# Performance work log

Measured on AMD Instinct MI355X. Metric: run time of the kernel, lower is better.

## Reference

```python
import jax, jax.numpy as jnp
import numpy as np
import math

CHUNK = 64

def _linear(x, W, b):
    # torch nn.Linear: y = x @ W.T + b
    return jnp.einsum('bsd,ed->bse', x, W) + b

def setup_inputs() -> dict:
    key = jax.random.key(0)
    ks = jax.random.split(key, 10)
    B, S, D = 4, 4096, 512
    scale = 0.02
    inp = {
        'x': jax.random.normal(ks[0], (B, S, D), jnp.float32),
        'base_phases': jax.random.normal(ks[1], (S, D), jnp.float32) * math.pi,
        'Wk': jax.random.normal(ks[2], (D, D), jnp.float32) * scale,
        'bk': jnp.zeros((D,), jnp.float32),
        'Wv': jax.random.normal(ks[3], (D, D), jnp.float32) * scale,
        'bv': jnp.zeros((D,), jnp.float32),
        'Wq': jax.random.normal(ks[4], (D, D), jnp.float32) * scale,
        'bq': jnp.zeros((D,), jnp.float32),
        'Wkm': jax.random.normal(ks[5], (D, D), jnp.float32) * scale,
        'bkm': jnp.zeros((D,), jnp.float32),
        'Wqm': jax.random.normal(ks[6], (D, D), jnp.float32) * scale,
        'bqm': jnp.zeros((D,), jnp.float32),
        'mod_scale': jnp.ones((1,), jnp.float32) * 0.1,
        'ln_g': jnp.ones((D,), jnp.float32),
        'ln_b': jnp.zeros((D,), jnp.float32),
        'Wo': jax.random.normal(ks[7], (D, D), jnp.float32) * scale,
        'bo': jnp.zeros((D,), jnp.float32),
    }
    return inp

def reference(x, base_phases, Wk, bk, Wv, bv, Wq, bq, Wkm, bkm, Wqm, bqm, mod_scale, ln_g, ln_b, Wo, bo):
    B, S, D = x.shape
    bp = base_phases[:S][None]                      # [1,S,D]
    key = _linear(x, Wk, bk)
    value = _linear(x, Wv, bv)
    query = _linear(x, Wq, bq)
    key_phase = bp + _linear(key, Wkm, bkm) * mod_scale
    query_phase = bp + _linear(query, Wqm, bqm) * mod_scale
    bound_real = value * jnp.cos(key_phase)
    bound_imag = value * jnp.sin(key_phase)
    # chunked cumulative memory (S divisible by CHUNK -> no padding)
    nC = S // CHUNK
    br = bound_real.reshape(B, nC, CHUNK, D)
    bi = bound_imag.reshape(B, nC, CHUNK, D)
    qp = query_phase.reshape(B, nC, CHUNK, D)
    mem_real = jnp.cumsum(br, axis=2)
    mem_imag = jnp.cumsum(bi, axis=2)
    retrieved = (mem_real * jnp.cos(qp) + mem_imag * jnp.sin(qp)).reshape(B, S, D)
    retrieved = retrieved / math.sqrt(D)
    # LayerNorm + Linear (to_out)
    mu = jnp.mean(retrieved, axis=-1, keepdims=True)
    var = jnp.mean((retrieved - mu) ** 2, axis=-1, keepdims=True)
    normed = (retrieved - mu) / jnp.sqrt(var + 1e-5) * ln_g + ln_b
    out = _linear(normed, Wo, bo)
    return x + out
```

## Files before the change

### kernel.cpp

```cpp
#include <hip/hip_runtime.h>
#include <hip/hip_bf16.h>


typedef __attribute__((ext_vector_type(8))) short short8;
typedef __attribute__((ext_vector_type(4))) float f32x4;

#define M_TOK   16384
#define DIM     512
#define NCHUNK  64
#define RPAD    520

__device__ __forceinline__ void gll16(const void* g, void* l) {
  __builtin_amdgcn_global_load_lds(
      (const __attribute__((address_space(1))) unsigned int*)g,
      (__attribute__((address_space(3))) unsigned int*)l, 16, 0, 0);
}

__device__ __forceinline__ uint2 pack4bf(float4 v) {
  union { __hip_bfloat16 h[4]; uint2 u; } t;
  t.h[0] = __float2bfloat16(v.x);
  t.h[1] = __float2bfloat16(v.y);
  t.h[2] = __float2bfloat16(v.z);
  t.h[3] = __float2bfloat16(v.w);
  return t.u;
}

__device__ __forceinline__ unsigned int pack2bf(float a, float b) {
  union { __hip_bfloat16 h[2]; unsigned int u; } t;
  t.h[0] = __float2bfloat16(a);
  t.h[1] = __float2bfloat16(b);
  return t.u;
}

__device__ __forceinline__ float u2f(unsigned short u) {
  union { unsigned int i; float f; } t;
  t.i = (unsigned int)u << 16;
  return t.f;
}

__global__ __launch_bounds__(256) void prep_all(
    const float* __restrict__ x, __hip_bfloat16* __restrict__ x_bf,
    const float* __restrict__ Wv, const float* __restrict__ Wo,
    const float* __restrict__ bv,
    const float* __restrict__ Wkm, const float* __restrict__ Wqm,
    const float* __restrict__ Wk, const float* __restrict__ Wq,
    const float* __restrict__ bk, const float* __restrict__ bkm,
    const float* __restrict__ bq, const float* __restrict__ bqm,
    __hip_bfloat16* __restrict__ Wall, float* __restrict__ bc1,
    __hip_bfloat16* __restrict__ Wm_bf, __hip_bfloat16* __restrict__ WT_bf) {
  const int tid = threadIdx.x;
  if (blockIdx.x < 8192) {
    int i = blockIdx.x * 256 + tid;
    ((uint2*)x_bf)[i] = pack4bf(((const float4*)x)[i]);
    return;
  }
  const int b = blockIdx.x - 8192;
  if (b < 512) {
    int m = b >> 8;
    int idx = ((b & 255) * 256 + tid) * 4;
    const float* src = m ? Wo : Wv;
    __hip_bfloat16* dst = Wall + (m ? (size_t)1536 * 512 : 0);
    ((uint2*)dst)[idx >> 2] = pack4bf(*(const float4*)(src + idx));
    int t = b * 256 + tid;
    if (t < 512) bc1[t] = bv[t];
  } else if (b < 1024) {
    int bb = b - 512;
    int m = bb >> 8;
    int idx = ((bb & 255) * 256 + tid) * 4;
    const float* src = m ? Wqm : Wkm;
    ((uint2*)(Wm_bf + (size_t)m * 262144))[idx >> 2] =
        pack4bf(*(const float4*)(src + idx));
  } else if (b < 1152) {
    __shared__ float tile[64][65];
    int bb = b - 1024;
    int z = bb >> 6;
    int tl = bb & 63;
    int tr = tl >> 3, tc = tl & 7;
    const float* src = z ? Wq : Wk;
#pragma unroll
    for (int i = 0; i < 4; i++) {
      int r = (tid >> 4) + 16 * i;
      int c4 = (tid & 15) * 4;
      float4 v = *(const float4*)(src + (size_t)(tr * 64 + r) * 512 +
                                  tc * 64 + c4);
      tile[r][c4 + 0] = v.x;
      tile[r][c4 + 1] = v.y;
      tile[r][c4 + 2] = v.z;
      tile[r][c4 + 3] = v.w;
    }
    __syncthreads();
    int orow = tid >> 2;
    int seg = tid & 3;
    __hip_bfloat16* dst = WT_bf + (size_t)z * 262144 +
                          (size_t)(tc * 64 + orow) * 512 + tr * 64 + seg * 16;
#pragma unroll
    for (int q = 0; q < 4; q++) {
      float4 v;
      v.x = tile[seg * 16 + q * 4 + 0][orow];
      v.y = tile[seg * 16 + q * 4 + 1][orow];
      v.z = tile[seg * 16 + q * 4 + 2][orow];
      v.w = tile[seg * 16 + q * 4 + 3][orow];
      *(uint2*)(dst + q * 4) = pack4bf(v);
    }
  } else {
    int row = (b - 1152) * 4 + (tid >> 6);
    int lane = tid & 63;
    int z = row >> 9;
    int i = row & 511;
    const float* Wm = z ? Wqm : Wkm;
    const float* b0 = z ? bq : bk;
    const float* bm = z ? bqm : bkm;
    const float4* w4 = (const float4*)(Wm + (size_t)i * 512 + lane * 8);
    const float4* v4 = (const float4*)(b0 + lane * 8);
    float4 w0 = w4[0], w1 = w4[1], c0 = v4[0], c1 = v4[1];
    float acc = w0.x * c0.x + w0.y * c0.y + w0.z * c0.z + w0.w * c0.w +
                w1.x * c1.x + w1.y * c1.y + w1.z * c1.z + w1.w * c1.w;
#pragma unroll
    for (int off = 32; off; off >>= 1) acc += __shfl_xor(acc, off, 64);
    if (lane == 0) bc1[512 + z * 512 + i] = acc + bm[i];
  }
}

__global__ __launch_bounds__(256) void gemm_bt(
    const __hip_bfloat16* __restrict__ A, int lda,
    const __hip_bfloat16* __restrict__ Bt,
    const float* __restrict__ bias,
    __hip_bfloat16* __restrict__ Cout, int ldc) {
  constexpr int K = 512, BK = 32;
  __shared__ __align__(16) __hip_bfloat16 As[2][128 * BK];
  __shared__ __align__(16) __hip_bfloat16 Bs[2][128 * BK];

  const int tid  = threadIdx.x;
  const int lane = tid & 63;
  const int w    = tid >> 6;
  const int wm   = w >> 1;
  const int wn   = w & 1;
  const int lb = (blockIdx.x & 7) * 192 + (blockIdx.x >> 3);
  const int by = lb / 12;
  const int bx = lb - by * 12;
  const int m0 = by * 128;
  const int n0 = bx * 128;

  const int rS0    = (w * 2 + 0) * 16 + (lane >> 2);
  const int rS1    = (w * 2 + 1) * 16 + (lane >> 2);
  const int kInRow = (lane & 3) * 8;
  const __hip_bfloat16* gA0 = A + (size_t)(m0 + rS0) * lda + kInRow;
  const __hip_bfloat16* gA1 = A + (size_t)(m0 + rS1) * lda + kInRow;
  const __hip_bfloat16* gB0 = Bt + (size_t)(n0 + rS0) * K + kInRow;
  const __hip_bfloat16* gB1 = Bt + (size_t)(n0 + rS1) * K + kInRow;
  char* ldsA0 = (char*)&As[0][0] + (w * 2 + 0) * 1024;
  char* ldsA1 = (char*)&As[0][0] + (w * 2 + 1) * 1024;
  char* ldsB0 = (char*)&Bs[0][0] + (w * 2 + 0) * 1024;
  char* ldsB1 = (char*)&Bs[0][0] + (w * 2 + 1) * 1024;

  f32x4 acc[4][4] = {};

  const int rfA = lane & 15;
  const int rfK = (lane >> 4) * 8;

  for (int kt = 0; kt < K; kt += 2 * BK) {
    __syncthreads();
    gll16(gA0 + kt, ldsA0);
    gll16(gA1 + kt, ldsA1);
    gll16(gB0 + kt, ldsB0);
    gll16(gB1 + kt, ldsB1);
    gll16(gA0 + kt + BK, ldsA0 + 8192);
    gll16(gA1 + kt + BK, ldsA1 + 8192);
    gll16(gB0 + kt + BK, ldsB0 + 8192);
    gll16(gB1 + kt + BK, ldsB1 + 8192);
    __syncthreads();

#pragma unroll
    for (int h = 0; h < 2; h++) {
      const __hip_bfloat16* Ah = &As[h][0];
      const __hip_bfloat16* Bh = &Bs[h][0];
      short8 af[4], bfv[4];
#pragma unroll
      for (int i = 0; i < 4; i++)
        af[i] = *(const short8*)(Ah + (wm * 64 + i * 16 + rfA) * BK + rfK);
#pragma unroll
      for (int j = 0; j < 4; j++)
        bfv[j] = *(const short8*)(Bh + (wn * 64 + j * 16 + rfA) * BK + rfK);
#pragma unroll
      for (int i = 0; i < 4; i++)
#pragma unroll
        for (int j = 0; j < 4; j++)
          acc[i][j] = __builtin_amdgcn_mfma_f32_16x16x32_bf16(
              af[i], bfv[j], acc[i][j], 0, 0, 0);
    }
  }

  const int cq = lane >> 4;
#pragma unroll
  for (int i = 0; i < 4; i++) {
    int row = m0 + wm * 64 + i * 16 + cq * 4;
#pragma unroll
    for (int j = 0; j < 4; j++) {
      int col = n0 + wn * 64 + j * 16 + (lane & 15);
      float bz = bias[col];
#pragma unroll
      for (int r = 0; r < 4; r++) {
        float v = acc[i][j][r] + bz;
        Cout[(size_t)(row + r) * ldc + col] = __float2bfloat16(v);
      }
    }
  }
}

__global__ __launch_bounds__(256) void gemm_compose(
    const __hip_bfloat16* __restrict__ Wm_bf,
    const __hip_bfloat16* __restrict__ WT_bf,
    __hip_bfloat16* __restrict__ Wall) {
  constexpr int K = 512, BK = 32;
  const __hip_bfloat16* A  = Wm_bf + (size_t)blockIdx.z * 262144;
  const __hip_bfloat16* Bt = WT_bf + (size_t)blockIdx.z * 262144;
  __hip_bfloat16* C = Wall + (size_t)(512 + blockIdx.z * 512) * 512;
  __shared__ __align__(16) __hip_bfloat16 As[128 * BK];
  __shared__ __align__(16) __hip_bfloat16 Bs[128 * BK];

  const int tid  = threadIdx.x;
  const int lane = tid & 63;
  const int w    = tid >> 6;
  const int wm   = w >> 1;
  const int wn   = w & 1;
  const int m0   = blockIdx.y * 128;
  const int n0   = blockIdx.x * 128;

  const int rS0    = (w * 2 + 0) * 16 + (lane >> 2);
  const int rS1    = (w * 2 + 1) * 16 + (lane >> 2);
  const int kInRow = (lane & 3) * 8;
  const __hip_bfloat16* gA0 = A + (size_t)(m0 + rS0) * K + kInRow;
  const __hip_bfloat16* gA1 = A + (size_t)(m0 + rS1) * K + kInRow;
  const __hip_bfloat16* gB0 = Bt + (size_t)(n0 + rS0) * K + kInRow;
  const __hip_bfloat16* gB1 = Bt + (size_t)(n0 + rS1) * K + kInRow;
  char* ldsA0 = (char*)As + (w * 2 + 0) * 1024;
  char* ldsA1 = (char*)As + (w * 2 + 1) * 1024;
  char* ldsB0 = (char*)Bs + (w * 2 + 0) * 1024;
  char* ldsB1 = (char*)Bs + (w * 2 + 1) * 1024;

  f32x4 acc[4][4] = {};
  const int rfA = lane & 15;
  const int rfK = (lane >> 4) * 8;

  for (int kt = 0; kt < K; kt += BK) {
    __syncthreads();
    gll16(gA0 + kt, ldsA0);
    gll16(gA1 + kt, ldsA1);
    gll16(gB0 + kt, ldsB0);
    gll16(gB1 + kt, ldsB1);
    __syncthreads();

    short8 af[4], bf[4];
#pragma unroll
    for (int i = 0; i < 4; i++)
      af[i] = *(const short8*)(As + (wm * 64 + i * 16 + rfA) * BK + rfK);
#pragma unroll
    for (int j = 0; j < 4; j++)
      bf[j] = *(const short8*)(Bs + (wn * 64 + j * 16 + rfA) * BK + rfK);
#pragma unroll
    for (int i = 0; i < 4; i++)
#pragma unroll
      for (int j = 0; j < 4; j++)
        acc[i][j] = __builtin_amdgcn_mfma_f32_16x16x32_bf16(
            af[i], bf[j], acc[i][j], 0, 0, 0);
  }

  const int cq = lane >> 4;
#pragma unroll
  for (int i = 0; i < 4; i++) {
    int row = m0 + wm * 64 + i * 16 + cq * 4;
#pragma unroll
    for (int j = 0; j < 4; j++) {
      int col = n0 + wn * 64 + j * 16 + (lane & 15);
#pragma unroll
      for (int r = 0; r < 4; r++)
        C[(size_t)(row + r) * 512 + col] = __float2bfloat16(acc[i][j][r]);
    }
  }
}

__global__ __launch_bounds__(1024) void fused_pg(
    const __hip_bfloat16* __restrict__ VKQ,
    const float* __restrict__ bp,
    const float* __restrict__ mod_scale,
    const float* __restrict__ ln_g, const float* __restrict__ ln_b,
    const __hip_bfloat16* __restrict__ WoB,
    const float* __restrict__ bo,
    const float* __restrict__ x,
    float* __restrict__ out) {
  __shared__ __hip_bfloat16 R[64 * RPAD];
  __shared__ float Tr[3][512], Ti[3][512];
  const int tid    = threadIdx.x;
  const int seg    = tid >> 8;
  const int d0     = (tid & 255) * 2;
  const int blk    = blockIdx.x;
  const int token0 = blk * 64;
  const int sg0    = (blk & (NCHUNK - 1)) * 64;
  const float msc  = mod_scale[0];
  const float isd  = 0.044194173824159216f;

  float cqs0[16], sqs0[16], cqs1[16], sqs1[16];

  {
    const int r0 = seg * 16;
    float mr0 = 0.f, mi0 = 0.f, mr1 = 0.f, mi1 = 0.f;
    const __hip_bfloat16* vb = VKQ + (size_t)(token0 + r0) * 1536 + d0;
    const float* bb = bp + (size_t)(sg0 + r0) * 512 + d0;
#pragma unroll
    for (int s = 0; s < 16; ++s) {
      ushort2 v2  = *(const ushort2*)(vb + (size_t)s * 1536);
      ushort2 km2 = *(const ushort2*)(vb + (size_t)s * 1536 + 512);
      ushort2 qm2 = *(const ushort2*)(vb + (size_t)s * 1536 + 1024);
      float2 b2   = *(const float2*)(bb + (size_t)s * 512);
      float v0 = u2f((unsigned short)v2.x), v1 = u2f((unsigned short)v2.y);
      float kp0 = b2.x + u2f((unsigned short)km2.x) * msc;
      float kp1 = b2.y + u2f((unsigned short)km2.y) * msc;
      float qp0 = b2.x + u2f((unsigned short)qm2.x) * msc;
      float qp1 = b2.y + u2f((unsigned short)qm2.y) * msc;
      float sk0, ck0, sk1, ck1, sq0, cq0, sq1, cq1;
      __sincosf(kp0, &sk0, &ck0);
      __sincosf(kp1, &sk1, &ck1);
      __sincosf(qp0, &sq0, &cq0);
      __sincosf(qp1, &sq1, &cq1);
      mr0 += v0 * ck0; mi0 += v0 * sk0;
      mr1 += v1 * ck1; mi1 += v1 * sk1;
      cqs0[s] = cq0; sqs0[s] = sq0;
      cqs1[s] = cq1; sqs1[s] = sq1;
      float rr0 = (mr0 * cq0 + mi0 * sq0) * isd;
      float rr1 = (mr1 * cq1 + mi1 * sq1) * isd;
      *(unsigned int*)(&R[(r0 + s) * RPAD + d0]) = pack2bf(rr0, rr1);
    }
    if (seg < 3) {
      Tr[seg][d0] = mr0; Tr[seg][d0 + 1] = mr1;
      Ti[seg][d0] = mi0; Ti[seg][d0 + 1] = mi1;
    }
  }
  __syncthreads();

  if (seg) {
    float pr0 = Tr[0][d0],     pi0 = Ti[0][d0];
    float pr1 = Tr[0][d0 + 1], pi1 = Ti[0][d0 + 1];
    if (seg >= 2) {
      pr0 += Tr[1][d0];     pi0 += Ti[1][d0];
      pr1 += Tr[1][d0 + 1]; pi1 += Ti[1][d0 + 1];
    }
    if (seg == 3) {
      pr0 += Tr[2][d0];     pi0 += Ti[2][d0];
      pr1 += Tr[2][d0 + 1]; pi1 += Ti[2][d0 + 1];
    }
    pr0 *= isd; pi0 *= isd; pr1 *= isd; pi1 *= isd;
    const int r0 = seg * 16;
#pragma unroll
    for (int s = 0; s < 16; ++s) {
      unsigned int* p = (unsigned int*)(&R[(r0 + s) * RPAD + d0]);
      unsigned int old = *p;
      float a = u2f((unsigned short)(old & 0xffffu)) +
                pr0 * cqs0[s] + pi0 * sqs0[s];
      float b = u2f((unsigned short)(old >> 16)) +
                pr1 * cqs1[s] + pi1 * sqs1[s];
      *p = pack2bf(a, b);
    }
  }
  __syncthreads();

  const int lane = tid & 63;
  const int wv   = tid >> 6;
  float xv[4][2][4];

  {
    float gj[8], bj[8];
#pragma unroll
    for (int j = 0; j < 8; j++) {
      int col = lane + 64 * j;
      gj[j] = ln_g[col];
      bj[j] = ln_b[col];
    }
    {
      const int cq_ = lane >> 4;
      const int c0  = lane & 15;
#pragma unroll
      for (int i = 0; i < 4; i++)
#pragma unroll
        for (int j = 0; j < 2; j++)
#pragma unroll
          for (int r = 0; r < 4; r++)
            xv[i][j][r] = x[(size_t)(token0 + i * 16 + cq_ * 4 + r) * 512 +
                            wv * 32 + j * 16 + c0];
    }
    for (int rr = 0; rr < 4; ++rr) {
      int row = wv * 4 + rr;
      float vals[8], sum = 0.f, sq2 = 0.f;
#pragma unroll
      for (int j = 0; j < 8; j++) {
        float v = u2f(*(const unsigned short*)&R[row * RPAD + lane + 64 * j]);
        vals[j] = v;
        sum += v;
        sq2 += v * v;
      }
#pragma unroll
      for (int off = 32; off; off >>= 1) {
        sum += __shfl_xor(sum, off, 64);
        sq2 += __shfl_xor(sq2, off, 64);
      }
      float mu   = sum * (1.f / 512.f);
      float var  = sq2 * (1.f / 512.f) - mu * mu;
      float rstd = rsqrtf(var + 1e-5f);
#pragma unroll
      for (int j = 0; j < 8; j++) {
        float nv = (vals[j] - mu) * rstd * gj[j] + bj[j];
        R[row * RPAD + lane + 64 * j] = __float2bfloat16(nv);
      }
    }
  }
  __syncthreads();

  {
    const int rfA = lane & 15;
    const int rfK = (lane >> 4) * 8;
    f32x4 acc[4][2] = {};

    for (int kt = 0; kt < 512; kt += 32) {
      short8 af[4], bfv[2];
#pragma unroll
      for (int j = 0; j < 2; j++) {
        int col = wv * 32 + j * 16 + rfA;
        bfv[j] = *(const short8*)(WoB + (size_t)col * 512 + kt + rfK);
      }
#pragma unroll
      for (int i = 0; i < 4; i++)
        af[i] = *(const short8*)(R + (i * 16 + rfA) * RPAD + kt + rfK);
#pragma unroll
      for (int i = 0; i < 4; i++)
#pragma unroll
        for (int j = 0; j < 2; j++)
          acc[i][j] = __builtin_amdgcn_mfma_f32_16x16x32_bf16(
              af[i], bfv[j], acc[i][j], 0, 0, 0);
    }

    const int cq_ = lane >> 4;
    float bz[2];
#pragma unroll
    for (int j = 0; j < 2; j++) bz[j] = bo[wv * 32 + j * 16 + (lane & 15)];
#pragma unroll
    for (int i = 0; i < 4; i++) {
      int row = token0 + i * 16 + cq_ * 4;
#pragma unroll
      for (int j = 0; j < 2; j++) {
        int col = wv * 32 + j * 16 + (lane & 15);
#pragma unroll
        for (int r = 0; r < 4; r++) {
          size_t o = (size_t)(row + r) * 512 + col;
          out[o] = acc[i][j][r] + bz[j] + xv[i][j][r];
        }
      }
    }
  }
}

extern "C" void kernel_launch(void* const* d_in, const int* in_sizes, int n_in,
                              void* d_out, int out_size, void* d_ws,
                              size_t ws_size, hipStream_t stream) {
  const float* x    = (const float*)d_in[0];
  const float* bp   = (const float*)d_in[1];
  const float* Wk   = (const float*)d_in[2];
  const float* bk   = (const float*)d_in[3];
  const float* Wv   = (const float*)d_in[4];
  const float* bv   = (const float*)d_in[5];
  const float* Wq   = (const float*)d_in[6];
  const float* bq   = (const float*)d_in[7];
  const float* Wkm  = (const float*)d_in[8];
  const float* bkm  = (const float*)d_in[9];
  const float* Wqm  = (const float*)d_in[10];
  const float* bqm  = (const float*)d_in[11];
  const float* msc  = (const float*)d_in[12];
  const float* lng  = (const float*)d_in[13];
  const float* lnb  = (const float*)d_in[14];
  const float* Wo   = (const float*)d_in[15];
  const float* bo   = (const float*)d_in[16];
  float* out = (float*)d_out;

  char* ws = (char*)d_ws;
  __hip_bfloat16* x_bf  = (__hip_bfloat16*)ws;  ws += (size_t)M_TOK * DIM * 2;
  __hip_bfloat16* Wall  = (__hip_bfloat16*)ws;  ws += (size_t)2048 * 512 * 2;
  __hip_bfloat16* Wm_bf = (__hip_bfloat16*)ws;  ws += (size_t)2 * 262144 * 2;
  __hip_bfloat16* WT_bf = (__hip_bfloat16*)ws;  ws += (size_t)2 * 262144 * 2;
  float*          bc1   = (float*)ws;           ws += 1536 * 4;
  __hip_bfloat16* VKQ   = (__hip_bfloat16*)ws;  ws += (size_t)M_TOK * 1536 * 2;

  prep_all<<<9600, 256, 0, stream>>>(x, x_bf, Wv, Wo, bv, Wkm, Wqm, Wk, Wq,
                                     bk, bkm, bq, bqm, Wall, bc1, Wm_bf,
                                     WT_bf);
  gemm_compose<<<dim3(4, 4, 2), 256, 0, stream>>>(Wm_bf, WT_bf, Wall);
  gemm_bt<<<dim3(1536), 256, 0, stream>>>(x_bf, DIM, Wall, bc1, VKQ, 1536);
  fused_pg<<<256, 1024, 0, stream>>>(VKQ, bp, msc, lng, lnb,
                                     Wall + (size_t)1536 * 512, bo, x, out);
}
```

Baseline: 202.3 us.

## Widen projection GEMM tile, overlap x conversion with compose, recompute query sincos

The main projection GEMM now uses 512-thread blocks computing 128x256 tiles (768 blocks instead of 1536), so A-tile loads are shared across more output columns. The x-to-bf16 conversion moves out of prep_all into the compose kernel, letting the small weight-composition GEMM blocks run alongside the conversion blocks. In fused_pg the per-thread arrays of query cos/sin are dropped and recomputed in the second pass, trading extra loads and sincos work for lower register pressure. The larger GEMM block raises LDS and register use per block and may reduce occupancy.

```diff
diff --git a/kernel.cpp b/kernel.cpp
--- a/kernel.cpp
+++ b/kernel.cpp
@@ -39,7 +39,6 @@
 }
 
 __global__ __launch_bounds__(256) void prep_all(
-    const float* __restrict__ x, __hip_bfloat16* __restrict__ x_bf,
     const float* __restrict__ Wv, const float* __restrict__ Wo,
     const float* __restrict__ bv,
     const float* __restrict__ Wkm, const float* __restrict__ Wqm,
@@ -49,12 +48,7 @@
     __hip_bfloat16* __restrict__ Wall, float* __restrict__ bc1,
     __hip_bfloat16* __restrict__ Wm_bf, __hip_bfloat16* __restrict__ WT_bf) {
   const int tid = threadIdx.x;
-  if (blockIdx.x < 8192) {
-    int i = blockIdx.x * 256 + tid;
-    ((uint2*)x_bf)[i] = pack4bf(((const float4*)x)[i]);
-    return;
-  }
-  const int b = blockIdx.x - 8192;
+  const int b = blockIdx.x;
   if (b < 512) {
     int m = b >> 8;
     int idx = ((b & 255) * 256 + tid) * 4;
@@ -121,110 +115,35 @@
   }
 }
 
-__global__ __launch_bounds__(256) void gemm_bt(
-    const __hip_bfloat16* __restrict__ A, int lda,
-    const __hip_bfloat16* __restrict__ Bt,
-    const float* __restrict__ bias,
-    __hip_bfloat16* __restrict__ Cout, int ldc) {
+__global__ __launch_bounds__(256) void compose_cvt(
+    const float* __restrict__ x, __hip_bfloat16* __restrict__ x_bf,
+    const __hip_bfloat16* __restrict__ Wm_bf,
+    const __hip_bfloat16* __restrict__ WT_bf,
+    __hip_bfloat16* __restrict__ Wall) {
   constexpr int K = 512, BK = 32;
-  __shared__ __align__(16) __hip_bfloat16 As[2][128 * BK];
-  __shared__ __align__(16) __hip_bfloat16 Bs[2][128 * BK];
-
-  const int tid  = threadIdx.x;
+  __shared__ __align__(16) __hip_bfloat16 As[128 * BK];
+  __shared__ __align__(16) __hip_bfloat16 Bs[128 * BK];
+
+  const int tid = threadIdx.x;
+  if (blockIdx.x < 8192) {
+    int i = blockIdx.x * 256 + tid;
+    ((uint2*)x_bf)[i] = pack4bf(((const float4*)x)[i]);
+    return;
+  }
+  const int b  = blockIdx.x - 8192;
+  const int z  = b >> 4;
+  const int by = (b >> 2) & 3;
+  const int bx = b & 3;
+  const __hip_bfloat16* A  = Wm_bf + (size_t)z * 262144;
+  const __hip_bfloat16* Bt = WT_bf + (size_t)z * 262144;
+  __hip_bfloat16* C = Wall + (size_t)(512 + z * 512) * 512;
+
   const int lane = tid & 63;
   const int w    = tid >> 6;
   const int wm   = w >> 1;
   const int wn   = w & 1;
-  const int lb = (blockIdx.x & 7) * 192 + (blockIdx.x >> 3);
-  const int by = lb / 12;
-  const int bx = lb - by * 12;
-  const int m0 = by * 128;
-  const int n0 = bx * 128;
-
-  const int rS0    = (w * 2 + 0) * 16 + (lane >> 2);
-  const int rS1    = (w * 2 + 1) * 16 + (lane >> 2);
-  const int kInRow = (lane & 3) * 8;
-  const __hip_bfloat16* gA0 = A + (size_t)(m0 + rS0) * lda + kInRow;
-  const __hip_bfloat16* gA1 = A + (size_t)(m0 + rS1) * lda + kInRow;
-  const __hip_bfloat16* gB0 = Bt + (size_t)(n0 + rS0) * K + kInRow;
-  const __hip_bfloat16* gB1 = Bt + (size_t)(n0 + rS1) * K + kInRow;
-  char* ldsA0 = (char*)&As[0][0] + (w * 2 + 0) * 1024;
-  char* ldsA1 = (char*)&As[0][0] + (w * 2 + 1) * 1024;
-  char* ldsB0 = (char*)&Bs[0][0] + (w * 2 + 0) * 1024;
-  char* ldsB1 = (char*)&Bs[0][0] + (w * 2 + 1) * 1024;
-
-  f32x4 acc[4][4] = {};
-
-  const int rfA = lane & 15;
-  const int rfK = (lane >> 4) * 8;
-
-  for (int kt = 0; kt < K; kt += 2 * BK) {
-    __syncthreads();
-    gll16(gA0 + kt, ldsA0);
-    gll16(gA1 + kt, ldsA1);
-    gll16(gB0 + kt, ldsB0);
-    gll16(gB1 + kt, ldsB1);
-    gll16(gA0 + kt + BK, ldsA0 + 8192);
-    gll16(gA1 + kt + BK, ldsA1 + 8192);
-    gll16(gB0 + kt + BK, ldsB0 + 8192);
-    gll16(gB1 + kt + BK, ldsB1 + 8192);
-    __syncthreads();
-
-#pragma unroll
-    for (int h = 0; h < 2; h++) {
-      const __hip_bfloat16* Ah = &As[h][0];
-      const __hip_bfloat16* Bh = &Bs[h][0];
-      short8 af[4], bfv[4];
-#pragma unroll
-      for (int i = 0; i < 4; i++)
-        af[i] = *(const short8*)(Ah + (wm * 64 + i * 16 + rfA) * BK + rfK);
-#pragma unroll
-      for (int j = 0; j < 4; j++)
-        bfv[j] = *(const short8*)(Bh + (wn * 64 + j * 16 + rfA) * BK + rfK);
-#pragma unroll
-      for (int i = 0; i < 4; i++)
-#pragma unroll
-        for (int j = 0; j < 4; j++)
-          acc[i][j] = __builtin_amdgcn_mfma_f32_16x16x32_bf16(
-              af[i], bfv[j], acc[i][j], 0, 0, 0);
-    }
-  }
-
-  const int cq = lane >> 4;
-#pragma unroll
-  for (int i = 0; i < 4; i++) {
-    int row = m0 + wm * 64 + i * 16 + cq * 4;
-#pragma unroll
-    for (int j = 0; j < 4; j++) {
-      int col = n0 + wn * 64 + j * 16 + (lane & 15);
-      float bz = bias[col];
-#pragma unroll
-      for (int r = 0; r < 4; r++) {
-        float v = acc[i][j][r] + bz;
-        Cout[(size_t)(row + r) * ldc + col] = __float2bfloat16(v);
-      }
-    }
-  }
-}
-
-__global__ __launch_bounds__(256) void gemm_compose(
-    const __hip_bfloat16* __restrict__ Wm_bf,
-    const __hip_bfloat16* __restrict__ WT_bf,
-    __hip_bfloat16* __restrict__ Wall) {
-  constexpr int K = 512, BK = 32;
-  const __hip_bfloat16* A  = Wm_bf + (size_t)blockIdx.z * 262144;
-  const __hip_bfloat16* Bt = WT_bf + (size_t)blockIdx.z * 262144;
-  __hip_bfloat16* C = Wall + (size_t)(512 + blockIdx.z * 512) * 512;
-  __shared__ __align__(16) __hip_bfloat16 As[128 * BK];
-  __shared__ __align__(16) __hip_bfloat16 Bs[128 * BK];
-
-  const int tid  = threadIdx.x;
-  const int lane = tid & 63;
-  const int w    = tid >> 6;
-  const int wm   = w >> 1;
-  const int wn   = w & 1;
-  const int m0   = blockIdx.y * 128;
-  const int n0   = blockIdx.x * 128;
+  const int m0   = by * 128;
+  const int n0   = bx * 128;
 
   const int rS0    = (w * 2 + 0) * 16 + (lane >> 2);
   const int rS1    = (w * 2 + 1) * 16 + (lane >> 2);
@@ -275,6 +194,87 @@
 #pragma unroll
       for (int r = 0; r < 4; r++)
         C[(size_t)(row + r) * 512 + col] = __float2bfloat16(acc[i][j][r]);
+    }
+  }
+}
+
+__global__ __launch_bounds__(512) void gemm_bt(
+    const __hip_bfloat16* __restrict__ A, int lda,
+    const __hip_bfloat16* __restrict__ Bt,
+    const float* __restrict__ bias,
+    __hip_bfloat16* __restrict__ Cout, int ldc) {
+  constexpr int K = 512, BK = 32;
+  __shared__ __align__(16) __hip_bfloat16 As[2][128 * BK];
+  __shared__ __align__(16) __hip_bfloat16 Bs[2][256 * BK];
+
+  const int tid  = threadIdx.x;
+  const int lane = tid & 63;
+  const int w    = tid >> 6;
+  const int wm   = w >> 2;
+  const int wn   = w & 3;
+  const int lb = (blockIdx.x & 7) * 96 + (blockIdx.x >> 3);
+  const int by = lb / 6;
+  const int bx = lb - by * 6;
+  const int m0 = by * 128;
+  const int n0 = bx * 256;
+
+  const int rS  = tid >> 2;
+  const int kIn = (tid & 3) * 8;
+  const __hip_bfloat16* gA  = A  + (size_t)(m0 + rS) * lda + kIn;
+  const __hip_bfloat16* gB0 = Bt + (size_t)(n0 + rS) * K + kIn;
+  const __hip_bfloat16* gB1 = Bt + (size_t)(n0 + 128 + rS) * K + kIn;
+  char* ldsA  = (char*)&As[0][0] + w * 1024;
+  char* ldsB0 = (char*)&Bs[0][0] + w * 1024;
+  char* ldsB1 = (char*)&Bs[0][0] + 8192 + w * 1024;
+
+  f32x4 acc[4][4] = {};
+
+  const int rfA = lane & 15;
+  const int rfK = (lane >> 4) * 8;
+
+  for (int kt = 0; kt < K; kt += 2 * BK) {
+    __syncthreads();
+    gll16(gA + kt, ldsA);
+    gll16(gB0 + kt, ldsB0);
+    gll16(gB1 + kt, ldsB1);
+    gll16(gA + kt + BK, ldsA + 8192);
+    gll16(gB0 + kt + BK, ldsB0 + 16384);
+    gll16(gB1 + kt + BK, ldsB1 + 16384);
+    __syncthreads();
+
+#pragma unroll
+    for (int h = 0; h < 2; h++) {
+      const __hip_bfloat16* Ah = &As[h][0];
+      const __hip_bfloat16* Bh = &Bs[h][0];
+      short8 af[4], bfv[4];
+#pragma unroll
+      for (int i = 0; i < 4; i++)
+        af[i] = *(const short8*)(Ah + (wm * 64 + i * 16 + rfA) * BK + rfK);
+#pragma unroll
+      for (int j = 0; j < 4; j++)
+        bfv[j] = *(const short8*)(Bh + (wn * 64 + j * 16 + rfA) * BK + rfK);
+#pragma unroll
+      for (int i = 0; i < 4; i++)
+#pragma unroll
+        for (int j = 0; j < 4; j++)
+          acc[i][j] = __builtin_amdgcn_mfma_f32_16x16x32_bf16(
+              af[i], bfv[j], acc[i][j], 0, 0, 0);
+    }
+  }
+
+  const int cq = lane >> 4;
+#pragma unroll
+  for (int i = 0; i < 4; i++) {
+    int row = m0 + wm * 64 + i * 16 + cq * 4;
+#pragma unroll
+    for (int j = 0; j < 4; j++) {
+      int col = n0 + wn * 64 + j * 16 + (lane & 15);
+      float bz = bias[col];
+#pragma unroll
+      for (int r = 0; r < 4; r++) {
+        float v = acc[i][j][r] + bz;
+        Cout[(size_t)(row + r) * ldc + col] = __float2bfloat16(v);
+      }
     }
   }
 }
@@ -299,8 +299,6 @@
   const float msc  = mod_scale[0];
   const float isd  = 0.044194173824159216f;
 
-  float cqs0[16], sqs0[16], cqs1[16], sqs1[16];
-
   {
     const int r0 = seg * 16;
     float mr0 = 0.f, mi0 = 0.f, mr1 = 0.f, mi1 = 0.f;
@@ -312,11 +310,11 @@
       ushort2 km2 = *(const ushort2*)(vb + (size_t)s * 1536 + 512);
       ushort2 qm2 = *(const ushort2*)(vb + (size_t)s * 1536 + 1024);
       float2 b2   = *(const float2*)(bb + (size_t)s * 512);
-      float v0 = u2f((unsigned short)v2.x), v1 = u2f((unsigned short)v2.y);
-      float kp0 = b2.x + u2f((unsigned short)km2.x) * msc;
-      float kp1 = b2.y + u2f((unsigned short)km2.y) * msc;
-      float qp0 = b2.x + u2f((unsigned short)qm2.x) * msc;
-      float qp1 = b2.y + u2f((unsigned short)qm2.y) * msc;
+      float v0 = u2f(v2.x), v1 = u2f(v2.y);
+      float kp0 = b2.x + u2f(km2.x) * msc;
+      float kp1 = b2.y + u2f(km2.y) * msc;
+      float qp0 = b2.x + u2f(qm2.x) * msc;
+      float qp1 = b2.y + u2f(qm2.y) * msc;
       float sk0, ck0, sk1, ck1, sq0, cq0, sq1, cq1;
       __sincosf(kp0, &sk0, &ck0);
       __sincosf(kp1, &sk1, &ck1);
@@ -324,8 +322,6 @@
       __sincosf(qp1, &sq1, &cq1);
       mr0 += v0 * ck0; mi0 += v0 * sk0;
       mr1 += v1 * ck1; mi1 += v1 * sk1;
-      cqs0[s] = cq0; sqs0[s] = sq0;
-      cqs1[s] = cq1; sqs1[s] = sq1;
       float rr0 = (mr0 * cq0 + mi0 * sq0) * isd;
       float rr1 = (mr1 * cq1 + mi1 * sq1) * isd;
       *(unsigned int*)(&R[(r0 + s) * RPAD + d0]) = pack2bf(rr0, rr1);
@@ -350,14 +346,21 @@
     }
     pr0 *= isd; pi0 *= isd; pr1 *= isd; pi1 *= isd;
     const int r0 = seg * 16;
+    const __hip_bfloat16* qb = VKQ + (size_t)(token0 + r0) * 1536 + 1024 + d0;
+    const float* bb = bp + (size_t)(sg0 + r0) * 512 + d0;
 #pragma unroll
     for (int s = 0; s < 16; ++s) {
+      ushort2 qm2 = *(const ushort2*)(qb + (size_t)s * 1536);
+      float2 b2   = *(const float2*)(bb + (size_t)s * 512);
+      float qp0 = b2.x + u2f(qm2.x) * msc;
+      float qp1 = b2.y + u2f(qm2.y) * msc;
+      float sq0, cq0, sq1, cq1;
+      __sincosf(qp0, &sq0, &cq0);
+      __sincosf(qp1, &sq1, &cq1);
       unsigned int* p = (unsigned int*)(&R[(r0 + s) * RPAD + d0]);
       unsigned int old = *p;
-      float a = u2f((unsigned short)(old & 0xffffu)) +
-                pr0 * cqs0[s] + pi0 * sqs0[s];
-      float b = u2f((unsigned short)(old >> 16)) +
-                pr1 * cqs1[s] + pi1 * sqs1[s];
+      float a = u2f((unsigned short)(old & 0xffffu)) + pr0 * cq0 + pi0 * sq0;
+      float b = u2f((unsigned short)(old >> 16))     + pr1 * cq1 + pi1 * sq1;
       *p = pack2bf(a, b);
     }
   }
@@ -392,7 +395,7 @@
       float vals[8], sum = 0.f, sq2 = 0.f;
 #pragma unroll
       for (int j = 0; j < 8; j++) {
-        float v = u2f(*(const unsigned short*)&R[row * RPAD + lane + 64 * j]);
+        float v = __bfloat162float(R[row * RPAD + lane + 64 * j]);
         vals[j] = v;
         sum += v;
         sq2 += v * v;
@@ -420,11 +423,11 @@
     f32x4 acc[4][2] = {};
 
     for (int kt = 0; kt < 512; kt += 32) {
-      short8 af[4], bfv[2];
+      short8 af[4], bf[2];
 #pragma unroll
       for (int j = 0; j < 2; j++) {
         int col = wv * 32 + j * 16 + rfA;
-        bfv[j] = *(const short8*)(WoB + (size_t)col * 512 + kt + rfK);
+        bf[j] = *(const short8*)(WoB + (size_t)col * 512 + kt + rfK);
       }
 #pragma unroll
       for (int i = 0; i < 4; i++)
@@ -434,7 +437,7 @@
 #pragma unroll
         for (int j = 0; j < 2; j++)
           acc[i][j] = __builtin_amdgcn_mfma_f32_16x16x32_bf16(
-              af[i], bfv[j], acc[i][j], 0, 0, 0);
+              af[i], bf[j], acc[i][j], 0, 0, 0);
     }
 
     const int cq_ = lane >> 4;
@@ -487,11 +490,11 @@
   float*          bc1   = (float*)ws;           ws += 1536 * 4;
   __hip_bfloat16* VKQ   = (__hip_bfloat16*)ws;  ws += (size_t)M_TOK * 1536 * 2;
 
-  prep_all<<<9600, 256, 0, stream>>>(x, x_bf, Wv, Wo, bv, Wkm, Wqm, Wk, Wq,
+  prep_all<<<1408, 256, 0, stream>>>(Wv, Wo, bv, Wkm, Wqm, Wk, Wq,
                                      bk, bkm, bq, bqm, Wall, bc1, Wm_bf,
                                      WT_bf);
-  gemm_compose<<<dim3(4, 4, 2), 256, 0, stream>>>(Wm_bf, WT_bf, Wall);
-  gemm_bt<<<dim3(1536), 256, 0, stream>>>(x_bf, DIM, Wall, bc1, VKQ, 1536);
+  compose_cvt<<<8224, 256, 0, stream>>>(x, x_bf, Wm_bf, WT_bf, Wall);
+  gemm_bt<<<dim3(768), 512, 0, stream>>>(x_bf, DIM, Wall, bc1, VKQ, 1536);
   fused_pg<<<256, 1024, 0, stream>>>(VKQ, bp, msc, lng, lnb,
                                      Wall + (size_t)1536 * 512, bo, x, out);
 }
```

New measurement: 204.2 us. About the same (+0.9%).
